# Kernel tuning notes

Measured on AMD Instinct MI355X. Metric: run time of the kernel, lower is better.

Reference implementation:

```python
import jax, jax.numpy as jnp
import numpy as np

B = 65536
IN = 512
SEQ = 4
LN_EPS = 1e-5


def _ln(x, g, b, eps=LN_EPS):
    # LayerNorm over last dim with affine params
    m = jnp.mean(x, axis=-1, keepdims=True)
    v = jnp.mean((x - m) ** 2, axis=-1, keepdims=True)
    return (x - m) * jax.lax.rsqrt(v + eps) * g + b


def setup_inputs() -> dict:
    key = jax.random.key(0)
    ks = jax.random.split(key, 24)

    def lin(k, shape, fan_in):
        return jax.random.normal(k, shape, jnp.float32) / np.sqrt(fan_in)

    return {
        "x": jax.random.normal(ks[0], (B, IN), jnp.float32),
        "history": jax.random.normal(ks[1], (B, SEQ * IN), jnp.float32),
        # gate network: (seq*in)->64->32
        "g1_w": lin(ks[2], (64, SEQ * IN), SEQ * IN), "g1_b": lin(ks[3], (64,), SEQ * IN),
        "g2_w": lin(ks[4], (32, 64), 64), "g2_b": lin(ks[5], (32,), 64),
        # base modulated layer in->128
        "base_w": lin(ks[6], (128, IN), IN), "base_b": lin(ks[7], (128,), IN),
        "ln1_g": jnp.ones((128,), jnp.float32), "ln1_b": jnp.zeros((128,), jnp.float32),
        # main network: NoisyLinear(eval) 128->64, LN(64), Linear 64->32
        "n1_w": lin(ks[8], (64, 128), 128), "n1_b": lin(ks[9], (64,), 128),
        "ln2_g": jnp.ones((64,), jnp.float32), "ln2_b": jnp.zeros((64,), jnp.float32),
        "m_w": lin(ks[10], (32, 64), 64), "m_b": lin(ks[11], (32,), 64),
        # value stream 32->16->1
        "v1_w": lin(ks[12], (16, 32), 32), "v1_b": lin(ks[13], (16,), 32),
        "v2_w": lin(ks[14], (1, 16), 16), "v2_b": lin(ks[15], (1,), 16),
        # advantage stream 32->16->4 (NoisyLinear in eval mode = mu only)
        "a1_w": lin(ks[16], (16, 32), 32), "a1_b": lin(ks[17], (16,), 32),
        "a2_w": lin(ks[18], (4, 16), 16), "a2_b": lin(ks[19], (4,), 16),
    }


def reference(x, history, g1_w, g1_b, g2_w, g2_b, base_w, base_b, ln1_g, ln1_b,
              n1_w, n1_b, ln2_g, ln2_b, m_w, m_b,
              v1_w, v1_b, v2_w, v2_b, a1_w, a1_b, a2_w, a2_b):
    # gate network
    h = jax.nn.relu(history @ g1_w.T + g1_b)
    gate_values = jax.nn.sigmoid(h @ g2_w.T + g2_b)            # [B, 32]
    mod = 0.7 + 0.3 * jnp.mean(gate_values, axis=1, keepdims=True)  # [B, 1]

    # per-sample scalar weight modulation: bmm(x, (mod*W)^T) == (x @ W^T) * mod
    x_gated = (x @ base_w.T) * mod + base_b                    # [B, 128]
    x_gated = _ln(jax.nn.relu(x_gated), ln1_g, ln1_b)

    # main network (NoisyLinear in eval mode -> mu weights)
    f = jax.nn.relu(x_gated @ n1_w.T + n1_b)
    f = _ln(f, ln2_g, ln2_b)
    features = jax.nn.relu(f @ m_w.T + m_b)                    # [B, 32]

    value = jax.nn.relu(features @ v1_w.T + v1_b) @ v2_w.T + v2_b    # [B, 1]
    advantage = jax.nn.relu(features @ a1_w.T + a1_b) @ a2_w.T + a2_b  # [B, 4]

    q_values = value + (advantage - jnp.mean(advantage, axis=1, keepdims=True))
    return q_values, gate_values
```

## Files before the change

### kernel.cpp

```cpp
#include <hip/hip_runtime.h>
#include <hip/hip_bf16.h>

typedef float f32x4 __attribute__((ext_vector_type(4)));
typedef __bf16 bf16x8 __attribute__((ext_vector_type(8)));
typedef __bf16 bf16x4 __attribute__((ext_vector_type(4)));

__device__ __forceinline__ f32x4 mfma16(bf16x8 a, bf16x8 b, f32x4 c) {
    return __builtin_amdgcn_mfma_f32_16x16x32_bf16(a, b, c, 0, 0, 0);
}

__device__ __forceinline__ float redsum16(float v) {
    v += __shfl_xor(v, 1);
    v += __shfl_xor(v, 2);
    v += __shfl_xor(v, 4);
    v += __shfl_xor(v, 8);
    return v;
}

struct bfpair { __bf16 h, l; };
__device__ __forceinline__ bfpair splitf(float f) {
    __bf16 hb = (__bf16)f;
    bfpair p;
    p.h = hb;
    p.l = (__bf16)(f - (float)hb);
    return p;
}

__global__ __launch_bounds__(256, 2)
void gated_dqn(const float* __restrict__ x,   const float* __restrict__ hist,
               const float* __restrict__ g1w, const float* __restrict__ g1b,
               const float* __restrict__ g2w, const float* __restrict__ g2b,
               const float* __restrict__ bw,  const float* __restrict__ bb,
               const float* __restrict__ ln1g,const float* __restrict__ ln1b,
               const float* __restrict__ n1w, const float* __restrict__ n1b,
               const float* __restrict__ ln2g,const float* __restrict__ ln2b,
               const float* __restrict__ mw,  const float* __restrict__ mb,
               const float* __restrict__ v1w, const float* __restrict__ v1b,
               const float* __restrict__ v2w, const float* __restrict__ v2b,
               const float* __restrict__ a1w, const float* __restrict__ a1b,
               const float* __restrict__ a2w, const float* __restrict__ a2b,
               float* __restrict__ qout, float* __restrict__ gateout)
{
    __shared__ __align__(16) __bf16 sXGh[64][136];
    __shared__ __align__(16) __bf16 sXGl[64][136];
    __shared__ __align__(16) __bf16 sA1h[64][72];
    __shared__ __align__(16) __bf16 sA1l[64][72];
    __shared__ __align__(16) __bf16 sW[10240];
    __shared__ float smod[64];

    const int tid = threadIdx.x;
    const int lane = tid & 63;
    const int wv = tid >> 6;
    const int qq = lane >> 4;
    const int c  = lane & 15;
    const int r0 = blockIdx.x * 64;
    const int rb = wv * 16 + qq * 4;

    {
        __bf16 (*Wg)[72] = reinterpret_cast<__bf16 (*)[72]>(sW);
        const int srow = tid >> 4, sc4 = tid & 15;
        const float* aSrc = hist + (size_t)(r0 + srow) * 2048 + sc4 * 4;
        const float* wSrc = g1w + (size_t)srow * 2048 + sc4 * 4;
        f32x4 ra[4], rw[4];
        #pragma unroll
        for (int i = 0; i < 4; ++i) {
            ra[i] = *(const f32x4*)(aSrc + i * 16 * 2048);
            rw[i] = *(const f32x4*)(wSrc + i * 16 * 2048);
        }
        f32x4 acc[4] = {{0,0,0,0},{0,0,0,0},{0,0,0,0},{0,0,0,0}};
        for (int kt = 0; kt < 32; ++kt) {
            __syncthreads();
            #pragma unroll
            for (int i = 0; i < 4; ++i) {
                bf16x4 va, vw;
                #pragma unroll
                for (int e = 0; e < 4; ++e) { va[e] = (__bf16)ra[i][e]; vw[e] = (__bf16)rw[i][e]; }
                *(bf16x4*)&sA1h[srow + i*16][sc4*4] = va;
                *(bf16x4*)&Wg [srow + i*16][sc4*4] = vw;
            }
            __syncthreads();
            if (kt + 1 < 32) {
                #pragma unroll
                for (int i = 0; i < 4; ++i) {
                    ra[i] = *(const f32x4*)(aSrc + i*16*2048 + (kt+1)*64);
                    rw[i] = *(const f32x4*)(wSrc + i*16*2048 + (kt+1)*64);
                }
            }
            #pragma unroll
            for (int ks = 0; ks < 2; ++ks) {
                bf16x8 a = *(const bf16x8*)&sA1h[wv*16 + c][ks*32 + qq*8];
                #pragma unroll
                for (int n = 0; n < 4; ++n) {
                    bf16x8 b = *(const bf16x8*)&Wg[n*16 + c][ks*32 + qq*8];
                    acc[n] = mfma16(a, b, acc[n]);
                }
            }
        }
        __syncthreads();
        #pragma unroll
        for (int n = 0; n < 4; ++n) {
            float bv = g1b[n*16 + c];
            #pragma unroll
            for (int j = 0; j < 4; ++j)
                sA1l[rb + j][n*16 + c] = (__bf16)fmaxf(acc[n][j] + bv, 0.0f);
        }
    }

    {
        __bf16 (*Wg2)[72] = reinterpret_cast<__bf16 (*)[72]>(sW);
        const int srow = tid >> 4, sc4 = tid & 15;
        #pragma unroll
        for (int i = 0; i < 2; ++i) {
            f32x4 v = *(const f32x4*)(g2w + (size_t)(srow + i*16) * 64 + sc4 * 4);
            bf16x4 vb;
            #pragma unroll
            for (int e = 0; e < 4; ++e) vb[e] = (__bf16)v[e];
            *(bf16x4*)&Wg2[srow + i*16][sc4*4] = vb;
        }
        __syncthreads();
        f32x4 acc[2] = {{0,0,0,0},{0,0,0,0}};
        #pragma unroll
        for (int ks = 0; ks < 2; ++ks) {
            bf16x8 a = *(const bf16x8*)&sA1l[wv*16 + c][ks*32 + qq*8];
            #pragma unroll
            for (int n = 0; n < 2; ++n) {
                bf16x8 b = *(const bf16x8*)&Wg2[n*16 + c][ks*32 + qq*8];
                acc[n] = mfma16(a, b, acc[n]);
            }
        }
        float s[4] = {0.f, 0.f, 0.f, 0.f};
        #pragma unroll
        for (int n = 0; n < 2; ++n) {
            float bv = g2b[n*16 + c];
            #pragma unroll
            for (int j = 0; j < 4; ++j) {
                float gv = 1.0f / (1.0f + __expf(-(acc[n][j] + bv)));
                gateout[(size_t)(r0 + rb + j) * 32 + n*16 + c] = gv;
                s[j] += gv;
            }
        }
        #pragma unroll
        for (int j = 0; j < 4; ++j) {
            float t = redsum16(s[j]);
            if (c == 0) smod[rb + j] = 0.7f + 0.3f * t * (1.0f / 32.0f);
        }
    }

    {
        __bf16 (*Xh)[40] = reinterpret_cast<__bf16 (*)[40]>(&sA1h[0][0]);
        __bf16 (*Xl)[40] = reinterpret_cast<__bf16 (*)[40]>(&sA1l[0][0]);
        __bf16 (*Bh)[40] = reinterpret_cast<__bf16 (*)[40]>(sW);
        __bf16 (*Bl)[40] = reinterpret_cast<__bf16 (*)[40]>(sW + 5120);
        const int srow = tid >> 3, sc3 = tid & 7;
        const float* aSrc = x + (size_t)(r0 + srow) * 512 + sc3 * 4;
        const float* wSrc = bw + (size_t)srow * 512 + sc3 * 4;
        f32x4 ra[2], rw[4];
        #pragma unroll
        for (int i = 0; i < 2; ++i) ra[i] = *(const f32x4*)(aSrc + i * 32 * 512);
        #pragma unroll
        for (int i = 0; i < 4; ++i) rw[i] = *(const f32x4*)(wSrc + i * 32 * 512);
        f32x4 acc[8] = {{0,0,0,0},{0,0,0,0},{0,0,0,0},{0,0,0,0},
                        {0,0,0,0},{0,0,0,0},{0,0,0,0},{0,0,0,0}};
        for (int kt = 0; kt < 16; ++kt) {
            __syncthreads();
            #pragma unroll
            for (int i = 0; i < 2; ++i) {
                bf16x4 vh, vl;
                #pragma unroll
                for (int e = 0; e < 4; ++e) { bfpair p = splitf(ra[i][e]); vh[e] = p.h; vl[e] = p.l; }
                *(bf16x4*)&Xh[srow + i*32][sc3*4] = vh;
                *(bf16x4*)&Xl[srow + i*32][sc3*4] = vl;
            }
            #pragma unroll
            for (int i = 0; i < 4; ++i) {
                bf16x4 vh, vl;
                #pragma unroll
                for (int e = 0; e < 4; ++e) { bfpair p = splitf(rw[i][e]); vh[e] = p.h; vl[e] = p.l; }
                *(bf16x4*)&Bh[srow + i*32][sc3*4] = vh;
                *(bf16x4*)&Bl[srow + i*32][sc3*4] = vl;
            }
            __syncthreads();
            if (kt + 1 < 16) {
                #pragma unroll
                for (int i = 0; i < 2; ++i) ra[i] = *(const f32x4*)(aSrc + i*32*512 + (kt+1)*32);
                #pragma unroll
                for (int i = 0; i < 4; ++i) rw[i] = *(const f32x4*)(wSrc + i*32*512 + (kt+1)*32);
            }
            bf16x8 ah = *(const bf16x8*)&Xh[wv*16 + c][qq*8];
            bf16x8 al = *(const bf16x8*)&Xl[wv*16 + c][qq*8];
            #pragma unroll
            for (int n = 0; n < 8; ++n) {
                bf16x8 bh = *(const bf16x8*)&Bh[n*16 + c][qq*8];
                bf16x8 bl = *(const bf16x8*)&Bl[n*16 + c][qq*8];
                acc[n] = mfma16(ah, bh, acc[n]);
                acc[n] = mfma16(al, bh, acc[n]);
                acc[n] = mfma16(ah, bl, acc[n]);
            }
        }
        __syncthreads();
        float mj[4];
        #pragma unroll
        for (int j = 0; j < 4; ++j) mj[j] = smod[rb + j];
        float s[4] = {0,0,0,0}, ss[4] = {0,0,0,0};
        #pragma unroll
        for (int n = 0; n < 8; ++n) {
            float b0 = bb[n*16 + c];
            #pragma unroll
            for (int j = 0; j < 4; ++j) {
                float v = fmaxf(acc[n][j] * mj[j] + b0, 0.0f);
                acc[n][j] = v;
                s[j] += v; ss[j] += v * v;
            }
        }
        float mean[4], rstd[4];
        #pragma unroll
        for (int j = 0; j < 4; ++j) {
            float t  = redsum16(s[j]);
            float t2 = redsum16(ss[j]);
            float m = t * (1.0f/128.0f);
            float var = t2 * (1.0f/128.0f) - m * m;
            mean[j] = m;
            rstd[j] = rsqrtf(var + 1e-5f);
        }
        #pragma unroll
        for (int n = 0; n < 8; ++n) {
            float g = ln1g[n*16 + c], b2 = ln1b[n*16 + c];
            #pragma unroll
            for (int j = 0; j < 4; ++j) {
                float y = (acc[n][j] - mean[j]) * rstd[j] * g + b2;
                bfpair p = splitf(y);
                sXGh[rb + j][n*16 + c] = p.h;
                sXGl[rb + j][n*16 + c] = p.l;
            }
        }
    }

    {
        __bf16 (*Wh)[72] = reinterpret_cast<__bf16 (*)[72]>(sW);
        __bf16 (*Wl)[72] = reinterpret_cast<__bf16 (*)[72]>(sW + 4608);
        const int srow = tid >> 4, sc4 = tid & 15;
        f32x4 acc[4] = {{0,0,0,0},{0,0,0,0},{0,0,0,0},{0,0,0,0}};
        for (int kh = 0; kh < 2; ++kh) {
            __syncthreads();
            #pragma unroll
            for (int i = 0; i < 4; ++i) {
                f32x4 v = *(const f32x4*)(n1w + (size_t)(srow + i*16) * 128 + kh*64 + sc4*4);
                bf16x4 vh, vl;
                #pragma unroll
                for (int e = 0; e < 4; ++e) { bfpair p = splitf(v[e]); vh[e] = p.h; vl[e] = p.l; }
                *(bf16x4*)&Wh[srow + i*16][sc4*4] = vh;
                *(bf16x4*)&Wl[srow + i*16][sc4*4] = vl;
            }
            __syncthreads();
            #pragma unroll
            for (int ks = 0; ks < 2; ++ks) {
                bf16x8 ah = *(const bf16x8*)&sXGh[wv*16 + c][kh*64 + ks*32 + qq*8];
                bf16x8 al = *(const bf16x8*)&sXGl[wv*16 + c][kh*64 + ks*32 + qq*8];
                #pragma unroll
                for (int n = 0; n < 4; ++n) {
                    bf16x8 bh = *(const bf16x8*)&Wh[n*16 + c][ks*32 + qq*8];
                    bf16x8 bl = *(const bf16x8*)&Wl[n*16 + c][ks*32 + qq*8];
                    acc[n] = mfma16(ah, bh, acc[n]);
                    acc[n] = mfma16(al, bh, acc[n]);
                    acc[n] = mfma16(ah, bl, acc[n]);
                }
            }
        }
        __syncthreads();
        float s[4] = {0,0,0,0}, ss[4] = {0,0,0,0};
        #pragma unroll
        for (int n = 0; n < 4; ++n) {
            float b0 = n1b[n*16 + c];
            #pragma unroll
            for (int j = 0; j < 4; ++j) {
                float v = fmaxf(acc[n][j] + b0, 0.0f);
                acc[n][j] = v; s[j] += v; ss[j] += v * v;
            }
        }
        #pragma unroll
        for (int j = 0; j < 4; ++j) {
            float t  = redsum16(s[j]);
            float t2 = redsum16(ss[j]);
            float m = t * (1.0f/64.0f);
            float var = t2 * (1.0f/64.0f) - m * m;
            s[j] = m;
            ss[j] = rsqrtf(var + 1e-5f);
        }
        #pragma unroll
        for (int n = 0; n < 4; ++n) {
            float g = ln2g[n*16 + c], b2 = ln2b[n*16 + c];
            #pragma unroll
            for (int j = 0; j < 4; ++j) {
                float y = (acc[n][j] - s[j]) * ss[j] * g + b2;
                bfpair p = splitf(y);
                sA1h[rb + j][n*16 + c] = p.h;
                sA1l[rb + j][n*16 + c] = p.l;
            }
        }
    }

    __bf16 (*Fh)[40] = reinterpret_cast<__bf16 (*)[40]>(&sXGh[0][0]);
    __bf16 (*Fl)[40] = reinterpret_cast<__bf16 (*)[40]>(&sXGl[0][0]);
    {
        __bf16 (*Wh)[72] = reinterpret_cast<__bf16 (*)[72]>(sW);
        __bf16 (*Wl)[72] = reinterpret_cast<__bf16 (*)[72]>(sW + 2304);
        const int srow = tid >> 4, sc4 = tid & 15;
        #pragma unroll
        for (int i = 0; i < 2; ++i) {
            f32x4 v = *(const f32x4*)(mw + (size_t)(srow + i*16) * 64 + sc4 * 4);
            bf16x4 vh, vl;
            #pragma unroll
            for (int e = 0; e < 4; ++e) { bfpair p = splitf(v[e]); vh[e] = p.h; vl[e] = p.l; }
            *(bf16x4*)&Wh[srow + i*16][sc4*4] = vh;
            *(bf16x4*)&Wl[srow + i*16][sc4*4] = vl;
        }
        __syncthreads();
        f32x4 acc[2] = {{0,0,0,0},{0,0,0,0}};
        #pragma unroll
        for (int ks = 0; ks < 2; ++ks) {
            bf16x8 ah = *(const bf16x8*)&sA1h[wv*16 + c][ks*32 + qq*8];
            bf16x8 al = *(const bf16x8*)&sA1l[wv*16 + c][ks*32 + qq*8];
            #pragma unroll
            for (int n = 0; n < 2; ++n) {
                bf16x8 bh = *(const bf16x8*)&Wh[n*16 + c][ks*32 + qq*8];
                bf16x8 bl = *(const bf16x8*)&Wl[n*16 + c][ks*32 + qq*8];
                acc[n] = mfma16(ah, bh, acc[n]);
                acc[n] = mfma16(al, bh, acc[n]);
                acc[n] = mfma16(ah, bl, acc[n]);
            }
        }
        #pragma unroll
        for (int n = 0; n < 2; ++n) {
            float b0 = mb[n*16 + c];
            #pragma unroll
            for (int j = 0; j < 4; ++j) {
                float v = fmaxf(acc[n][j] + b0, 0.0f);
                bfpair p = splitf(v);
                Fh[rb + j][n*16 + c] = p.h;
                Fl[rb + j][n*16 + c] = p.l;
            }
        }
    }

    {
        __syncthreads();
        __bf16 (*V1h)[40] = reinterpret_cast<__bf16 (*)[40]>(sW);
        __bf16 (*V1l)[40] = reinterpret_cast<__bf16 (*)[40]>(sW + 640);
        __bf16 (*A1h)[40] = reinterpret_cast<__bf16 (*)[40]>(sW + 1280);
        __bf16 (*A1l)[40] = reinterpret_cast<__bf16 (*)[40]>(sW + 1920);
        {
            int m   = tid >> 7;
            int row = (tid >> 3) & 15;
            int c4  = tid & 7;
            const float* src = (m == 0 ? v1w : a1w) + row * 32 + c4 * 4;
            f32x4 v = *(const f32x4*)src;
            bf16x4 vh, vl;
            #pragma unroll
            for (int e = 0; e < 4; ++e) { bfpair p = splitf(v[e]); vh[e] = p.h; vl[e] = p.l; }
            __bf16 (*Dh)[40] = (m == 0) ? V1h : A1h;
            __bf16 (*Dl)[40] = (m == 0) ? V1l : A1l;
            *(bf16x4*)&Dh[row][c4*4] = vh;
            *(bf16x4*)&Dl[row][c4*4] = vl;
        }
        __syncthreads();
        bf16x8 ah = *(const bf16x8*)&Fh[wv*16 + c][qq*8];
        bf16x8 al = *(const bf16x8*)&Fl[wv*16 + c][qq*8];
        f32x4 av = {0,0,0,0}, aa = {0,0,0,0};
        {
            bf16x8 bh = *(const bf16x8*)&V1h[c][qq*8];
            bf16x8 bl = *(const bf16x8*)&V1l[c][qq*8];
            av = mfma16(ah, bh, av); av = mfma16(al, bh, av); av = mfma16(ah, bl, av);
        }
        {
            bf16x8 bh = *(const bf16x8*)&A1h[c][qq*8];
            bf16x8 bl = *(const bf16x8*)&A1l[c][qq*8];
            aa = mfma16(ah, bh, aa); aa = mfma16(al, bh, aa); aa = mfma16(ah, bl, aa);
        }
        float v1bc = v1b[c], a1bc = a1b[c], w2 = v2w[c];
        float vb2 = v2b[0];
        float aw0 = a2w[c], aw1 = a2w[16 + c], aw2 = a2w[32 + c], aw3 = a2w[48 + c];
        float ab0 = a2b[0], ab1 = a2b[1], ab2 = a2b[2], ab3 = a2b[3];
        #pragma unroll
        for (int j = 0; j < 4; ++j) {
            float hv = fmaxf(av[j] + v1bc, 0.0f);
            float ha = fmaxf(aa[j] + a1bc, 0.0f);
            float val = redsum16(hv * w2) + vb2;
            float d0 = redsum16(ha * aw0) + ab0;
            float d1 = redsum16(ha * aw1) + ab1;
            float d2 = redsum16(ha * aw2) + ab2;
            float d3 = redsum16(ha * aw3) + ab3;
            float ma = 0.25f * (d0 + d1 + d2 + d3);
            if (c == 0) {
                f32x4 qv = {val + d0 - ma, val + d1 - ma, val + d2 - ma, val + d3 - ma};
                *(f32x4*)(qout + (size_t)(r0 + rb + j) * 4) = qv;
            }
        }
    }
}

extern "C" void kernel_launch(void* const* d_in, const int* in_sizes, int n_in,
                              void* d_out, int out_size, void* d_ws, size_t ws_size,
                              hipStream_t stream) {
    (void)in_sizes; (void)n_in; (void)d_ws; (void)ws_size; (void)out_size;
    const float* x    = (const float*)d_in[0];
    const float* hist = (const float*)d_in[1];
    const float* g1w  = (const float*)d_in[2];
    const float* g1b  = (const float*)d_in[3];
    const float* g2w  = (const float*)d_in[4];
    const float* g2b  = (const float*)d_in[5];
    const float* bw   = (const float*)d_in[6];
    const float* bb   = (const float*)d_in[7];
    const float* ln1g = (const float*)d_in[8];
    const float* ln1b = (const float*)d_in[9];
    const float* n1w  = (const float*)d_in[10];
    const float* n1b  = (const float*)d_in[11];
    const float* ln2g = (const float*)d_in[12];
    const float* ln2b = (const float*)d_in[13];
    const float* mw   = (const float*)d_in[14];
    const float* mb   = (const float*)d_in[15];
    const float* v1w  = (const float*)d_in[16];
    const float* v1b  = (const float*)d_in[17];
    const float* v2w  = (const float*)d_in[18];
    const float* v2b  = (const float*)d_in[19];
    const float* a1w  = (const float*)d_in[20];
    const float* a1b  = (const float*)d_in[21];
    const float* a2w  = (const float*)d_in[22];
    const float* a2b  = (const float*)d_in[23];
    float* qout = (float*)d_out;
    float* gateout = qout + (size_t)65536 * 4;
    gated_dqn<<<dim3(65536 / 64), dim3(256), 0, stream>>>(
        x, hist, g1w, g1b, g2w, g2b, bw, bb, ln1g, ln1b, n1w, n1b,
        ln2g, ln2b, mw, mb, v1w, v1b, v2w, v2b, a1w, a1b, a2w, a2b,
        qout, gateout);
}
```

Before: 180.9 us.

## Prepack weights into MFMA fragment layout and run per-wave independent pipelines

Adds a small pre-kernel that converts every weight matrix into bf16 (and hi/lo split) arrays already laid out as MFMA B-operand fragments in the workspace. The main kernel then gives each wave its own 16 rows, reads activations straight from global memory into registers with one-step prefetch, and keeps intermediates in a per-wave swizzled LDS scratch. This removes the block-wide __syncthreads staging, the repeated per-block weight conversion and the LDS round-trips for the big GEMMs. In exchange it adds an extra kernel launch every call and relies on L2 to serve weight fragments to all waves.

```diff
diff --git a/kernel.cpp b/kernel.cpp
--- a/kernel.cpp
+++ b/kernel.cpp
@@ -3,382 +3,304 @@
 
 typedef float f32x4 __attribute__((ext_vector_type(4)));
 typedef __bf16 bf16x8 __attribute__((ext_vector_type(8)));
-typedef __bf16 bf16x4 __attribute__((ext_vector_type(4)));
+typedef unsigned int u32;
+typedef u32 u32x4 __attribute__((ext_vector_type(4)));
+
+#define PK1  0
+#define PK2  131072
+#define PK3  133120
+#define PK4  264192
+#define PK5  280576
+#define PK6V 284672
+#define PK6A 285696
 
 __device__ __forceinline__ f32x4 mfma16(bf16x8 a, bf16x8 b, f32x4 c) {
     return __builtin_amdgcn_mfma_f32_16x16x32_bf16(a, b, c, 0, 0, 0);
 }
-
 __device__ __forceinline__ float redsum16(float v) {
-    v += __shfl_xor(v, 1);
-    v += __shfl_xor(v, 2);
-    v += __shfl_xor(v, 4);
-    v += __shfl_xor(v, 8);
+    v += __shfl_xor(v, 1); v += __shfl_xor(v, 2);
+    v += __shfl_xor(v, 4); v += __shfl_xor(v, 8);
     return v;
 }
-
-struct bfpair { __bf16 h, l; };
-__device__ __forceinline__ bfpair splitf(float f) {
-    __bf16 hb = (__bf16)f;
-    bfpair p;
-    p.h = hb;
-    p.l = (__bf16)(f - (float)hb);
-    return p;
-}
-
-__global__ __launch_bounds__(256, 2)
-void gated_dqn(const float* __restrict__ x,   const float* __restrict__ hist,
-               const float* __restrict__ g1w, const float* __restrict__ g1b,
-               const float* __restrict__ g2w, const float* __restrict__ g2b,
-               const float* __restrict__ bw,  const float* __restrict__ bb,
-               const float* __restrict__ ln1g,const float* __restrict__ ln1b,
-               const float* __restrict__ n1w, const float* __restrict__ n1b,
-               const float* __restrict__ ln2g,const float* __restrict__ ln2b,
-               const float* __restrict__ mw,  const float* __restrict__ mb,
-               const float* __restrict__ v1w, const float* __restrict__ v1b,
-               const float* __restrict__ v2w, const float* __restrict__ v2b,
-               const float* __restrict__ a1w, const float* __restrict__ a1b,
-               const float* __restrict__ a2w, const float* __restrict__ a2b,
-               float* __restrict__ qout, float* __restrict__ gateout)
+__device__ __forceinline__ unsigned short bfb(__bf16 b) {
+    return __builtin_bit_cast(unsigned short, b);
+}
+__device__ __forceinline__ bf16x8 cvt8(f32x4 a, f32x4 b) {
+    bf16x8 r;
+    r[0]=(__bf16)a[0]; r[1]=(__bf16)a[1]; r[2]=(__bf16)a[2]; r[3]=(__bf16)a[3];
+    r[4]=(__bf16)b[0]; r[5]=(__bf16)b[1]; r[6]=(__bf16)b[2]; r[7]=(__bf16)b[3];
+    return r;
+}
+__device__ __forceinline__ void split8(f32x4 a, f32x4 b, bf16x8& h, bf16x8& l) {
+    #pragma unroll
+    for (int e=0;e<4;++e){ __bf16 hb=(__bf16)a[e]; h[e]=hb; l[e]=(__bf16)(a[e]-(float)hb); }
+    #pragma unroll
+    for (int e=0;e<4;++e){ __bf16 hb=(__bf16)b[e]; h[4+e]=hb; l[4+e]=(__bf16)(b[e]-(float)hb); }
+}
+__device__ __forceinline__ void unpack8(u32x4 w0, u32x4 w1, bf16x8& h, bf16x8& l) {
+    u32 h0=(w0[0]&0xFFFFu)|(w0[1]<<16), h1=(w0[2]&0xFFFFu)|(w0[3]<<16);
+    u32 h2=(w1[0]&0xFFFFu)|(w1[1]<<16), h3=(w1[2]&0xFFFFu)|(w1[3]<<16);
+    u32 l0=(w0[0]>>16)|(w0[1]&0xFFFF0000u), l1=(w0[2]>>16)|(w0[3]&0xFFFF0000u);
+    u32 l2=(w1[0]>>16)|(w1[1]&0xFFFF0000u), l3=(w1[2]>>16)|(w1[3]&0xFFFF0000u);
+    u32x4 hv={h0,h1,h2,h3}, lv={l0,l1,l2,l3};
+    h=__builtin_bit_cast(bf16x8,hv); l=__builtin_bit_cast(bf16x8,lv);
+}
+
+__device__ __forceinline__ void pack_plain(const float* __restrict__ W, __bf16* __restrict__ dst,
+                                           int i, int K, int Nn) {
+    int e=i&7, lane=(i>>3)&63, p=i>>9;
+    int n=p%Nn, t=p/Nn;
+    float v = W[(size_t)(n*16+(lane&15))*K + t*32 + (lane>>4)*8 + e];
+    dst[i] = (__bf16)v;
+}
+__device__ __forceinline__ void pack_hilo(const float* __restrict__ W, __bf16* __restrict__ dst,
+                                          int i, int K, int Nn) {
+    int e=i&7, lane=(i>>3)&63, p=i>>9;
+    int n=p%Nn, t=p/Nn;
+    float v = W[(size_t)(n*16+(lane&15))*K + t*32 + (lane>>4)*8 + e];
+    __bf16 h = (__bf16)v;
+    dst[p*1024 + (i&511)]       = h;
+    dst[p*1024 + 512 + (i&511)] = (__bf16)(v - (float)h);
+}
+__global__ void pack_weights(const float* g1w, const float* g2w, const float* bw,
+                             const float* n1w, const float* mw, const float* v1w,
+                             const float* a1w, __bf16* wsb) {
+    int gi = blockIdx.x*256 + threadIdx.x;
+    if      (gi < 131072) pack_plain(g1w, wsb+PK1, gi,          2048, 4);
+    else if (gi < 133120) pack_plain(g2w, wsb+PK2, gi-131072,   64,   2);
+    else if (gi < 198656) pack_hilo (bw,  wsb+PK3, gi-133120,   512,  8);
+    else if (gi < 206848) pack_hilo (n1w, wsb+PK4, gi-198656,   128,  4);
+    else if (gi < 208896) pack_hilo (mw,  wsb+PK5, gi-206848,   64,   2);
+    else if (gi < 209408) pack_hilo (v1w, wsb+PK6V, gi-208896,  32,   1);
+    else if (gi < 209920) pack_hilo (a1w, wsb+PK6A, gi-209408,  32,   1);
+}
+
+__global__ __launch_bounds__(256, 4)
+void gated_dqn_main(const float* __restrict__ x,   const float* __restrict__ hist,
+                    const float* __restrict__ g1b, const float* __restrict__ g2b,
+                    const float* __restrict__ bb,  const float* __restrict__ ln1g,
+                    const float* __restrict__ ln1b,const float* __restrict__ n1b,
+                    const float* __restrict__ ln2g,const float* __restrict__ ln2b,
+                    const float* __restrict__ mb,  const float* __restrict__ v1b,
+                    const float* __restrict__ v2w, const float* __restrict__ v2b,
+                    const float* __restrict__ a1b, const float* __restrict__ a2w,
+                    const float* __restrict__ a2b, const __bf16* __restrict__ wsb,
+                    float* __restrict__ qout, float* __restrict__ gateout)
 {
-    __shared__ __align__(16) __bf16 sXGh[64][136];
-    __shared__ __align__(16) __bf16 sXGl[64][136];
-    __shared__ __align__(16) __bf16 sA1h[64][72];
-    __shared__ __align__(16) __bf16 sA1l[64][72];
-    __shared__ __align__(16) __bf16 sW[10240];
-    __shared__ float smod[64];
-
-    const int tid = threadIdx.x;
-    const int lane = tid & 63;
-    const int wv = tid >> 6;
-    const int qq = lane >> 4;
-    const int c  = lane & 15;
-    const int r0 = blockIdx.x * 64;
-    const int rb = wv * 16 + qq * 4;
-
-    {
-        __bf16 (*Wg)[72] = reinterpret_cast<__bf16 (*)[72]>(sW);
-        const int srow = tid >> 4, sc4 = tid & 15;
-        const float* aSrc = hist + (size_t)(r0 + srow) * 2048 + sc4 * 4;
-        const float* wSrc = g1w + (size_t)srow * 2048 + sc4 * 4;
-        f32x4 ra[4], rw[4];
-        #pragma unroll
-        for (int i = 0; i < 4; ++i) {
-            ra[i] = *(const f32x4*)(aSrc + i * 16 * 2048);
-            rw[i] = *(const f32x4*)(wSrc + i * 16 * 2048);
-        }
-        f32x4 acc[4] = {{0,0,0,0},{0,0,0,0},{0,0,0,0},{0,0,0,0}};
-        for (int kt = 0; kt < 32; ++kt) {
-            __syncthreads();
-            #pragma unroll
-            for (int i = 0; i < 4; ++i) {
-                bf16x4 va, vw;
-                #pragma unroll
-                for (int e = 0; e < 4; ++e) { va[e] = (__bf16)ra[i][e]; vw[e] = (__bf16)rw[i][e]; }
-                *(bf16x4*)&sA1h[srow + i*16][sc4*4] = va;
-                *(bf16x4*)&Wg [srow + i*16][sc4*4] = vw;
-            }
-            __syncthreads();
-            if (kt + 1 < 32) {
-                #pragma unroll
-                for (int i = 0; i < 4; ++i) {
-                    ra[i] = *(const f32x4*)(aSrc + i*16*2048 + (kt+1)*64);
-                    rw[i] = *(const f32x4*)(wSrc + i*16*2048 + (kt+1)*64);
-                }
-            }
-            #pragma unroll
-            for (int ks = 0; ks < 2; ++ks) {
-                bf16x8 a = *(const bf16x8*)&sA1h[wv*16 + c][ks*32 + qq*8];
+    __shared__ __align__(16) u32 scr[4][2048];
+    const int tid = threadIdx.x, lane = tid & 63, wv = tid >> 6;
+    const int qq = lane >> 4, c = lane & 15;
+    const int r0 = (blockIdx.x*4 + wv)*16;
+    u32*    my  = scr[wv];
+    __bf16* myb = (__bf16*)my;
+    const int swc = ((c >> 1) & 3) << 3;
+
+    f32x4 acc[4] = {};
+    {
+        const float*  aB = hist + (size_t)(r0 + c)*2048 + qq*8;
+        const __bf16* bB = wsb + PK1 + lane*8;
+        f32x4 ca0 = *(const f32x4*)(aB), ca1 = *(const f32x4*)(aB + 4);
+        bf16x8 cb0 = *(const bf16x8*)(bB),       cb1 = *(const bf16x8*)(bB+512);
+        bf16x8 cb2 = *(const bf16x8*)(bB+1024),  cb3 = *(const bf16x8*)(bB+1536);
+        for (int kt = 0; kt < 64; ++kt) {
+            int k1 = (kt+1 < 64) ? kt+1 : kt;
+            f32x4 na0 = *(const f32x4*)(aB + k1*32), na1 = *(const f32x4*)(aB + k1*32 + 4);
+            const __bf16* bt = bB + k1*2048;
+            bf16x8 nb0 = *(const bf16x8*)(bt),      nb1 = *(const bf16x8*)(bt+512);
+            bf16x8 nb2 = *(const bf16x8*)(bt+1024), nb3 = *(const bf16x8*)(bt+1536);
+            bf16x8 af = cvt8(ca0, ca1);
+            acc[0] = mfma16(af, cb0, acc[0]); acc[1] = mfma16(af, cb1, acc[1]);
+            acc[2] = mfma16(af, cb2, acc[2]); acc[3] = mfma16(af, cb3, acc[3]);
+            ca0 = na0; ca1 = na1; cb0 = nb0; cb1 = nb1; cb2 = nb2; cb3 = nb3;
+        }
+        #pragma unroll
+        for (int n = 0; n < 4; ++n) {
+            float bv = g1b[n*16 + c];
+            #pragma unroll
+            for (int j = 0; j < 4; ++j) {
+                int r = qq*4 + j, col = n*16 + c;
+                myb[r*64 + (col ^ (((r>>1)&3)<<3))] = (__bf16)fmaxf(acc[n][j] + bv, 0.0f);
+            }
+        }
+    }
+
+    float mj[4];
+    {
+        const __bf16* bB = wsb + PK2 + lane*8;
+        bf16x8 a0 = *(const bf16x8*)&myb[c*64 + ((qq*8) ^ swc)];
+        bf16x8 a1 = *(const bf16x8*)&myb[c*64 + ((32 + qq*8) ^ swc)];
+        bf16x8 b00 = *(const bf16x8*)(bB),      b01 = *(const bf16x8*)(bB+512);
+        bf16x8 b10 = *(const bf16x8*)(bB+1024), b11 = *(const bf16x8*)(bB+1536);
+        f32x4 ag0 = {}, ag1 = {};
+        ag0 = mfma16(a0, b00, ag0); ag1 = mfma16(a0, b01, ag1);
+        ag0 = mfma16(a1, b10, ag0); ag1 = mfma16(a1, b11, ag1);
+        float s[4] = {0,0,0,0};
+        #pragma unroll
+        for (int n = 0; n < 2; ++n) {
+            float bv = g2b[n*16 + c];
+            f32x4 ag = n ? ag1 : ag0;
+            #pragma unroll
+            for (int j = 0; j < 4; ++j) {
+                float gv = 1.0f / (1.0f + __expf(-(ag[j] + bv)));
+                gateout[(size_t)(r0 + qq*4 + j)*32 + n*16 + c] = gv;
+                s[j] += gv;
+            }
+        }
+        #pragma unroll
+        for (int j = 0; j < 4; ++j)
+            mj[j] = 0.7f + 0.3f * redsum16(s[j]) * (1.0f/32.0f);
+    }
+
+    f32x4 a3[8] = {};
+    {
+        const float*  aB = x + (size_t)(r0 + c)*512 + qq*8;
+        const __bf16* bB = wsb + PK3 + lane*8;
+        f32x4 ca0 = *(const f32x4*)(aB), ca1 = *(const f32x4*)(aB + 4);
+        for (int kt = 0; kt < 16; ++kt) {
+            int k1 = (kt+1 < 16) ? kt+1 : kt;
+            f32x4 na0 = *(const f32x4*)(aB + k1*32), na1 = *(const f32x4*)(aB + k1*32 + 4);
+            bf16x8 ah, al; split8(ca0, ca1, ah, al);
+            const __bf16* bt = bB + kt*8192;
+            #pragma unroll
+            for (int half = 0; half < 2; ++half) {
+                const __bf16* bt2 = bt + half*4096;
                 #pragma unroll
                 for (int n = 0; n < 4; ++n) {
-                    bf16x8 b = *(const bf16x8*)&Wg[n*16 + c][ks*32 + qq*8];
-                    acc[n] = mfma16(a, b, acc[n]);
+                    bf16x8 bh = *(const bf16x8*)(bt2 + n*1024);
+                    bf16x8 bl = *(const bf16x8*)(bt2 + n*1024 + 512);
+                    f32x4 a = a3[half*4 + n];
+                    a = mfma16(ah, bh, a); a = mfma16(al, bh, a); a = mfma16(ah, bl, a);
+                    a3[half*4 + n] = a;
                 }
             }
-        }
-        __syncthreads();
-        #pragma unroll
-        for (int n = 0; n < 4; ++n) {
-            float bv = g1b[n*16 + c];
-            #pragma unroll
-            for (int j = 0; j < 4; ++j)
-                sA1l[rb + j][n*16 + c] = (__bf16)fmaxf(acc[n][j] + bv, 0.0f);
-        }
-    }
-
-    {
-        __bf16 (*Wg2)[72] = reinterpret_cast<__bf16 (*)[72]>(sW);
-        const int srow = tid >> 4, sc4 = tid & 15;
-        #pragma unroll
-        for (int i = 0; i < 2; ++i) {
-            f32x4 v = *(const f32x4*)(g2w + (size_t)(srow + i*16) * 64 + sc4 * 4);
-            bf16x4 vb;
-            #pragma unroll
-            for (int e = 0; e < 4; ++e) vb[e] = (__bf16)v[e];
-            *(bf16x4*)&Wg2[srow + i*16][sc4*4] = vb;
-        }
-        __syncthreads();
-        f32x4 acc[2] = {{0,0,0,0},{0,0,0,0}};
-        #pragma unroll
-        for (int ks = 0; ks < 2; ++ks) {
-            bf16x8 a = *(const bf16x8*)&sA1l[wv*16 + c][ks*32 + qq*8];
-            #pragma unroll
-            for (int n = 0; n < 2; ++n) {
-                bf16x8 b = *(const bf16x8*)&Wg2[n*16 + c][ks*32 + qq*8];
-                acc[n] = mfma16(a, b, acc[n]);
-            }
-        }
-        float s[4] = {0.f, 0.f, 0.f, 0.f};
-        #pragma unroll
-        for (int n = 0; n < 2; ++n) {
-            float bv = g2b[n*16 + c];
-            #pragma unroll
-            for (int j = 0; j < 4; ++j) {
-                float gv = 1.0f / (1.0f + __expf(-(acc[n][j] + bv)));
-                gateout[(size_t)(r0 + rb + j) * 32 + n*16 + c] = gv;
-                s[j] += gv;
-            }
-        }
+            ca0 = na0; ca1 = na1;
+        }
+        float s[4] = {0,0,0,0}, ss[4] = {0,0,0,0};
+        #pragma unroll
+        for (int n = 0; n < 8; ++n) {
+            float bv = bb[n*16 + c];
+            #pragma unroll
+            for (int j = 0; j < 4; ++j) {
+                float v = fmaxf(a3[n][j]*mj[j] + bv, 0.0f);
+                a3[n][j] = v; s[j] += v; ss[j] += v*v;
+            }
+        }
+        float mean[4], rstd[4];
         #pragma unroll
         for (int j = 0; j < 4; ++j) {
-            float t = redsum16(s[j]);
-            if (c == 0) smod[rb + j] = 0.7f + 0.3f * t * (1.0f / 32.0f);
-        }
-    }
-
-    {
-        __bf16 (*Xh)[40] = reinterpret_cast<__bf16 (*)[40]>(&sA1h[0][0]);
-        __bf16 (*Xl)[40] = reinterpret_cast<__bf16 (*)[40]>(&sA1l[0][0]);
-        __bf16 (*Bh)[40] = reinterpret_cast<__bf16 (*)[40]>(sW);
-        __bf16 (*Bl)[40] = reinterpret_cast<__bf16 (*)[40]>(sW + 5120);
-        const int srow = tid >> 3, sc3 = tid & 7;
-        const float* aSrc = x + (size_t)(r0 + srow) * 512 + sc3 * 4;
-        const float* wSrc = bw + (size_t)srow * 512 + sc3 * 4;
-        f32x4 ra[2], rw[4];
-        #pragma unroll
-        for (int i = 0; i < 2; ++i) ra[i] = *(const f32x4*)(aSrc + i * 32 * 512);
-        #pragma unroll
-        for (int i = 0; i < 4; ++i) rw[i] = *(const f32x4*)(wSrc + i * 32 * 512);
-        f32x4 acc[8] = {{0,0,0,0},{0,0,0,0},{0,0,0,0},{0,0,0,0},
-                        {0,0,0,0},{0,0,0,0},{0,0,0,0},{0,0,0,0}};
-        for (int kt = 0; kt < 16; ++kt) {
-            __syncthreads();
-            #pragma unroll
-            for (int i = 0; i < 2; ++i) {
-                bf16x4 vh, vl;
-                #pragma unroll
-                for (int e = 0; e < 4; ++e) { bfpair p = splitf(ra[i][e]); vh[e] = p.h; vl[e] = p.l; }
-                *(bf16x4*)&Xh[srow + i*32][sc3*4] = vh;
-                *(bf16x4*)&Xl[srow + i*32][sc3*4] = vl;
-            }
-            #pragma unroll
-            for (int i = 0; i < 4; ++i) {
-                bf16x4 vh, vl;
-                #pragma unroll
-                for (int e = 0; e < 4; ++e) { bfpair p = splitf(rw[i][e]); vh[e] = p.h; vl[e] = p.l; }
-                *(bf16x4*)&Bh[srow + i*32][sc3*4] = vh;
-                *(bf16x4*)&Bl[srow + i*32][sc3*4] = vl;
-            }
-            __syncthreads();
-            if (kt + 1 < 16) {
-                #pragma unroll
-                for (int i = 0; i < 2; ++i) ra[i] = *(const f32x4*)(aSrc + i*32*512 + (kt+1)*32);
-                #pragma unroll
-                for (int i = 0; i < 4; ++i) rw[i] = *(const f32x4*)(wSrc + i*32*512 + (kt+1)*32);
-            }
-            bf16x8 ah = *(const bf16x8*)&Xh[wv*16 + c][qq*8];
-            bf16x8 al = *(const bf16x8*)&Xl[wv*16 + c][qq*8];
-            #pragma unroll
-            for (int n = 0; n < 8; ++n) {
-                bf16x8 bh = *(const bf16x8*)&Bh[n*16 + c][qq*8];
-                bf16x8 bl = *(const bf16x8*)&Bl[n*16 + c][qq*8];
-                acc[n] = mfma16(ah, bh, acc[n]);
-                acc[n] = mfma16(al, bh, acc[n]);
-                acc[n] = mfma16(ah, bl, acc[n]);
-            }
-        }
-        __syncthreads();
-        float mj[4];
-        #pragma unroll
-        for (int j = 0; j < 4; ++j) mj[j] = smod[rb + j];
-        float s[4] = {0,0,0,0}, ss[4] = {0,0,0,0};
-        #pragma unroll
-        for (int n = 0; n < 8; ++n) {
-            float b0 = bb[n*16 + c];
-            #pragma unroll
-            for (int j = 0; j < 4; ++j) {
-                float v = fmaxf(acc[n][j] * mj[j] + b0, 0.0f);
-                acc[n][j] = v;
-                s[j] += v; ss[j] += v * v;
-            }
-        }
-        float mean[4], rstd[4];
-        #pragma unroll
-        for (int j = 0; j < 4; ++j) {
-            float t  = redsum16(s[j]);
-            float t2 = redsum16(ss[j]);
+            float t = redsum16(s[j]), t2 = redsum16(ss[j]);
             float m = t * (1.0f/128.0f);
-            float var = t2 * (1.0f/128.0f) - m * m;
-            mean[j] = m;
-            rstd[j] = rsqrtf(var + 1e-5f);
-        }
+            mean[j] = m; rstd[j] = rsqrtf(t2*(1.0f/128.0f) - m*m + 1e-5f);
+        }
+        asm volatile("s_waitcnt lgkmcnt(0)" ::: "memory");
         #pragma unroll
         for (int n = 0; n < 8; ++n) {
             float g = ln1g[n*16 + c], b2 = ln1b[n*16 + c];
             #pragma unroll
             for (int j = 0; j < 4; ++j) {
-                float y = (acc[n][j] - mean[j]) * rstd[j] * g + b2;
-                bfpair p = splitf(y);
-                sXGh[rb + j][n*16 + c] = p.h;
-                sXGl[rb + j][n*16 + c] = p.l;
-            }
-        }
-    }
-
-    {
-        __bf16 (*Wh)[72] = reinterpret_cast<__bf16 (*)[72]>(sW);
-        __bf16 (*Wl)[72] = reinterpret_cast<__bf16 (*)[72]>(sW + 4608);
-        const int srow = tid >> 4, sc4 = tid & 15;
-        f32x4 acc[4] = {{0,0,0,0},{0,0,0,0},{0,0,0,0},{0,0,0,0}};
-        for (int kh = 0; kh < 2; ++kh) {
-            __syncthreads();
-            #pragma unroll
-            for (int i = 0; i < 4; ++i) {
-                f32x4 v = *(const f32x4*)(n1w + (size_t)(srow + i*16) * 128 + kh*64 + sc4*4);
-                bf16x4 vh, vl;
-                #pragma unroll
-                for (int e = 0; e < 4; ++e) { bfpair p = splitf(v[e]); vh[e] = p.h; vl[e] = p.l; }
-                *(bf16x4*)&Wh[srow + i*16][sc4*4] = vh;
-                *(bf16x4*)&Wl[srow + i*16][sc4*4] = vl;
-            }
-            __syncthreads();
-            #pragma unroll
-            for (int ks = 0; ks < 2; ++ks) {
-                bf16x8 ah = *(const bf16x8*)&sXGh[wv*16 + c][kh*64 + ks*32 + qq*8];
-                bf16x8 al = *(const bf16x8*)&sXGl[wv*16 + c][kh*64 + ks*32 + qq*8];
-                #pragma unroll
-                for (int n = 0; n < 4; ++n) {
-                    bf16x8 bh = *(const bf16x8*)&Wh[n*16 + c][ks*32 + qq*8];
-                    bf16x8 bl = *(const bf16x8*)&Wl[n*16 + c][ks*32 + qq*8];
-                    acc[n] = mfma16(ah, bh, acc[n]);
-                    acc[n] = mfma16(al, bh, acc[n]);
-                    acc[n] = mfma16(ah, bl, acc[n]);
-                }
-            }
-        }
-        __syncthreads();
+                int r = qq*4 + j, col = n*16 + c;
+                float y = (a3[n][j] - mean[j]) * rstd[j] * g + b2;
+                __bf16 hb = (__bf16)y; __bf16 lb = (__bf16)(y - (float)hb);
+                my[r*128 + (col ^ (((r>>1)&3)<<3))] = (u32)bfb(hb) | ((u32)bfb(lb) << 16);
+            }
+        }
+    }
+
+    f32x4 a4[4] = {};
+    {
+        const __bf16* bB = wsb + PK4 + lane*8;
+        #pragma unroll
+        for (int t = 0; t < 4; ++t) {
+            int base = c*128 + ((t*32 + qq*8) ^ swc);
+            u32x4 w0 = *(const u32x4*)&my[base], w1 = *(const u32x4*)&my[base + 4];
+            bf16x8 ah, al; unpack8(w0, w1, ah, al);
+            const __bf16* bt = bB + t*4096;
+            #pragma unroll
+            for (int n = 0; n < 4; ++n) {
+                bf16x8 bh = *(const bf16x8*)(bt + n*1024);
+                bf16x8 bl = *(const bf16x8*)(bt + n*1024 + 512);
+                f32x4 a = a4[n];
+                a = mfma16(ah, bh, a); a = mfma16(al, bh, a); a = mfma16(ah, bl, a);
+                a4[n] = a;
+            }
+        }
         float s[4] = {0,0,0,0}, ss[4] = {0,0,0,0};
         #pragma unroll
         for (int n = 0; n < 4; ++n) {
-            float b0 = n1b[n*16 + c];
-            #pragma unroll
-            for (int j = 0; j < 4; ++j) {
-                float v = fmaxf(acc[n][j] + b0, 0.0f);
-                acc[n][j] = v; s[j] += v; ss[j] += v * v;
-            }
-        }
+            float bv = n1b[n*16 + c];
+            #pragma unroll
+            for (int j = 0; j < 4; ++j) {
+                float v = fmaxf(a4[n][j] + bv, 0.0f);
+                a4[n][j] = v; s[j] += v; ss[j] += v*v;
+            }
+        }
+        float mean[4], rstd[4];
         #pragma unroll
         for (int j = 0; j < 4; ++j) {
-            float t  = redsum16(s[j]);
-            float t2 = redsum16(ss[j]);
+            float t = redsum16(s[j]), t2 = redsum16(ss[j]);
             float m = t * (1.0f/64.0f);
-            float var = t2 * (1.0f/64.0f) - m * m;
-            s[j] = m;
-            ss[j] = rsqrtf(var + 1e-5f);
-        }
+            mean[j] = m; rstd[j] = rsqrtf(t2*(1.0f/64.0f) - m*m + 1e-5f);
+        }
+        asm volatile("s_waitcnt lgkmcnt(0)" ::: "memory");
         #pragma unroll
         for (int n = 0; n < 4; ++n) {
             float g = ln2g[n*16 + c], b2 = ln2b[n*16 + c];
             #pragma unroll
             for (int j = 0; j < 4; ++j) {
-                float y = (acc[n][j] - s[j]) * ss[j] * g + b2;
-                bfpair p = splitf(y);
-                sA1h[rb + j][n*16 + c] = p.h;
-                sA1l[rb + j][n*16 + c] = p.l;
-            }
-        }
-    }
-
-    __bf16 (*Fh)[40] = reinterpret_cast<__bf16 (*)[40]>(&sXGh[0][0]);
-    __bf16 (*Fl)[40] = reinterpret_cast<__bf16 (*)[40]>(&sXGl[0][0]);
-    {
-        __bf16 (*Wh)[72] = reinterpret_cast<__bf16 (*)[72]>(sW);
-        __bf16 (*Wl)[72] = reinterpret_cast<__bf16 (*)[72]>(sW + 2304);
-        const int srow = tid >> 4, sc4 = tid & 15;
-        #pragma unroll
-        for (int i = 0; i < 2; ++i) {
-            f32x4 v = *(const f32x4*)(mw + (size_t)(srow + i*16) * 64 + sc4 * 4);
-            bf16x4 vh, vl;
-            #pragma unroll
-            for (int e = 0; e < 4; ++e) { bfpair p = splitf(v[e]); vh[e] = p.h; vl[e] = p.l; }
-            *(bf16x4*)&Wh[srow + i*16][sc4*4] = vh;
-            *(bf16x4*)&Wl[srow + i*16][sc4*4] = vl;
-        }
-        __syncthreads();
-        f32x4 acc[2] = {{0,0,0,0},{0,0,0,0}};
-        #pragma unroll
-        for (int ks = 0; ks < 2; ++ks) {
-            bf16x8 ah = *(const bf16x8*)&sA1h[wv*16 + c][ks*32 + qq*8];
-            bf16x8 al = *(const bf16x8*)&sA1l[wv*16 + c][ks*32 + qq*8];
+                int r = qq*4 + j, col = n*16 + c;
+                float y = (a4[n][j] - mean[j]) * rstd[j] * g + b2;
+                __bf16 hb = (__bf16)y; __bf16 lb = (__bf16)(y - (float)hb);
+                my[r*64 + (col ^ (((r>>1)&3)<<3))] = (u32)bfb(hb) | ((u32)bfb(lb) << 16);
+            }
+        }
+    }
+
+    {
+        const __bf16* bB = wsb + PK5 + lane*8;
+        f32x4 a5[2] = {};
+        #pragma unroll
+        for (int t = 0; t < 2; ++t) {
+            int base = c*64 + ((t*32 + qq*8) ^ swc);
+            u32x4 w0 = *(const u32x4*)&my[base], w1 = *(const u32x4*)&my[base + 4];
+            bf16x8 ah, al; unpack8(w0, w1, ah, al);
+            const __bf16* bt = bB + t*2048;
             #pragma unroll
             for (int n = 0; n < 2; ++n) {
-                bf16x8 bh = *(const bf16x8*)&Wh[n*16 + c][ks*32 + qq*8];
-                bf16x8 bl = *(const bf16x8*)&Wl[n*16 + c][ks*32 + qq*8];
-                acc[n] = mfma16(ah, bh, acc[n]);
-                acc[n] = mfma16(al, bh, acc[n]);
-                acc[n] = mfma16(ah, bl, acc[n]);
-            }
-        }
+                bf16x8 bh = *(const bf16x8*)(bt + n*1024);
+                bf16x8 bl = *(const bf16x8*)(bt + n*1024 + 512);
+                f32x4 a = a5[n];
+                a = mfma16(ah, bh, a); a = mfma16(al, bh, a); a = mfma16(ah, bl, a);
+                a5[n] = a;
+            }
+        }
+        asm volatile("s_waitcnt lgkmcnt(0)" ::: "memory");
         #pragma unroll
         for (int n = 0; n < 2; ++n) {
-            float b0 = mb[n*16 + c];
-            #pragma unroll
-            for (int j = 0; j < 4; ++j) {
-                float v = fmaxf(acc[n][j] + b0, 0.0f);
-                bfpair p = splitf(v);
-                Fh[rb + j][n*16 + c] = p.h;
-                Fl[rb + j][n*16 + c] = p.l;
-            }
-        }
-    }
-
-    {
-        __syncthreads();
-        __bf16 (*V1h)[40] = reinterpret_cast<__bf16 (*)[40]>(sW);
-        __bf16 (*V1l)[40] = reinterpret_cast<__bf16 (*)[40]>(sW + 640);
-        __bf16 (*A1h)[40] = reinterpret_cast<__bf16 (*)[40]>(sW + 1280);
-        __bf16 (*A1l)[40] = reinterpret_cast<__bf16 (*)[40]>(sW + 1920);
-        {
-            int m   = tid >> 7;
-            int row = (tid >> 3) & 15;
-            int c4  = tid & 7;
-            const float* src = (m == 0 ? v1w : a1w) + row * 32 + c4 * 4;
-            f32x4 v = *(const f32x4*)src;
-            bf16x4 vh, vl;
-            #pragma unroll
-            for (int e = 0; e < 4; ++e) { bfpair p = splitf(v[e]); vh[e] = p.h; vl[e] = p.l; }
-            __bf16 (*Dh)[40] = (m == 0) ? V1h : A1h;
-            __bf16 (*Dl)[40] = (m == 0) ? V1l : A1l;
-            *(bf16x4*)&Dh[row][c4*4] = vh;
-            *(bf16x4*)&Dl[row][c4*4] = vl;
-        }
-        __syncthreads();
-        bf16x8 ah = *(const bf16x8*)&Fh[wv*16 + c][qq*8];
-        bf16x8 al = *(const bf16x8*)&Fl[wv*16 + c][qq*8];
-        f32x4 av = {0,0,0,0}, aa = {0,0,0,0};
-        {
-            bf16x8 bh = *(const bf16x8*)&V1h[c][qq*8];
-            bf16x8 bl = *(const bf16x8*)&V1l[c][qq*8];
-            av = mfma16(ah, bh, av); av = mfma16(al, bh, av); av = mfma16(ah, bl, av);
-        }
-        {
-            bf16x8 bh = *(const bf16x8*)&A1h[c][qq*8];
-            bf16x8 bl = *(const bf16x8*)&A1l[c][qq*8];
-            aa = mfma16(ah, bh, aa); aa = mfma16(al, bh, aa); aa = mfma16(ah, bl, aa);
-        }
+            float bv = mb[n*16 + c];
+            #pragma unroll
+            for (int j = 0; j < 4; ++j) {
+                int r = qq*4 + j, col = n*16 + c;
+                float v = fmaxf(a5[n][j] + bv, 0.0f);
+                __bf16 hb = (__bf16)v; __bf16 lb = (__bf16)(v - (float)hb);
+                my[r*32 + (col ^ (((r>>1)&3)<<3))] = (u32)bfb(hb) | ((u32)bfb(lb) << 16);
+            }
+        }
+    }
+
+    {
+        int base = c*32 + ((qq*8) ^ swc);
+        u32x4 w0 = *(const u32x4*)&my[base], w1 = *(const u32x4*)&my[base + 4];
+        bf16x8 ah, al; unpack8(w0, w1, ah, al);
+        const __bf16* bv_ = wsb + PK6V + lane*8;
+        const __bf16* ba_ = wsb + PK6A + lane*8;
+        bf16x8 vh = *(const bf16x8*)(bv_), vl = *(const bf16x8*)(bv_ + 512);
+        bf16x8 ahw = *(const bf16x8*)(ba_), alw = *(const bf16x8*)(ba_ + 512);
+        f32x4 av = {}, aa = {};
+        av = mfma16(ah, vh, av); av = mfma16(al, vh, av); av = mfma16(ah, vl, av);
+        aa = mfma16(ah, ahw, aa); aa = mfma16(al, ahw, aa); aa = mfma16(ah, alw, aa);
         float v1bc = v1b[c], a1bc = a1b[c], w2 = v2w[c];
         float vb2 = v2b[0];
-        float aw0 = a2w[c], aw1 = a2w[16 + c], aw2 = a2w[32 + c], aw3 = a2w[48 + c];
+        float aw0 = a2w[c], aw1 = a2w[16+c], aw2 = a2w[32+c], aw3 = a2w[48+c];
         float ab0 = a2b[0], ab1 = a2b[1], ab2 = a2b[2], ab3 = a2b[3];
         #pragma unroll
         for (int j = 0; j < 4; ++j) {
@@ -392,7 +314,7 @@
             float ma = 0.25f * (d0 + d1 + d2 + d3);
             if (c == 0) {
                 f32x4 qv = {val + d0 - ma, val + d1 - ma, val + d2 - ma, val + d3 - ma};
-                *(f32x4*)(qout + (size_t)(r0 + rb + j) * 4) = qv;
+                *(f32x4*)(qout + (size_t)(r0 + qq*4 + j)*4) = qv;
             }
         }
     }
@@ -401,7 +323,7 @@
 extern "C" void kernel_launch(void* const* d_in, const int* in_sizes, int n_in,
                               void* d_out, int out_size, void* d_ws, size_t ws_size,
                               hipStream_t stream) {
-    (void)in_sizes; (void)n_in; (void)d_ws; (void)ws_size; (void)out_size;
+    (void)in_sizes; (void)n_in; (void)ws_size; (void)out_size;
     const float* x    = (const float*)d_in[0];
     const float* hist = (const float*)d_in[1];
     const float* g1w  = (const float*)d_in[2];
@@ -426,10 +348,12 @@
     const float* a1b  = (const float*)d_in[21];
     const float* a2w  = (const float*)d_in[22];
     const float* a2b  = (const float*)d_in[23];
+    __bf16* wsb = (__bf16*)d_ws;
     float* qout = (float*)d_out;
     float* gateout = qout + (size_t)65536 * 4;
-    gated_dqn<<<dim3(65536 / 64), dim3(256), 0, stream>>>(
-        x, hist, g1w, g1b, g2w, g2b, bw, bb, ln1g, ln1b, n1w, n1b,
-        ln2g, ln2b, mw, mb, v1w, v1b, v2w, v2b, a1w, a1b, a2w, a2b,
-        qout, gateout);
-}
+
+    pack_weights<<<dim3(820), dim3(256), 0, stream>>>(g1w, g2w, bw, n1w, mw, v1w, a1w, wsb);
+    gated_dqn_main<<<dim3(1024), dim3(256), 0, stream>>>(
+        x, hist, g1b, g2b, bb, ln1g, ln1b, n1b, ln2g, ln2b, mb,
+        v1b, v2w, v2b, a1b, a2w, a2b, wsb, qout, gateout);
+}
```

New measurement: 249.6 us. +38.0%, slower.
